# Kernel optimization log

Measured on AMD Instinct MI355X. Metric: run time of the kernel, lower is better.

## Reference

```python
import jax, jax.numpy as jnp
import numpy as np

D = 256
B, N1, N2 = 4, 512, 512


def setup_inputs() -> dict:
    key = jax.random.key(0)
    k = jax.random.split(key, 6)
    s1 = 1.0 / np.sqrt(2 * D)  # torch Linear init bound ~ U(-1/sqrt(fan_in), ...)
    s2 = 1.0 / np.sqrt(D)
    return {
        "x": jax.random.normal(k[0], (B, N1, D), jnp.float32),
        "y": jax.random.normal(k[1], (B, N2, D), jnp.float32),
        "W1": jax.random.uniform(k[2], (2 * D, D), jnp.float32, -s1, s1),  # linear1.weight.T
        "b1": jax.random.uniform(k[3], (D,), jnp.float32, -s1, s1),
        "W2": jax.random.uniform(k[4], (D, 1), jnp.float32, -s2, s2),  # out.weight.T
        "b2": jax.random.uniform(k[5], (1,), jnp.float32, -s2, s2),
    }


def reference(x, y, W1, b1, W2, b2):
    # linear1 over concat([x,y]) is separable: split W1 into x-part and y-part,
    # project each sequence once, then broadcast-sum over the (n1, n2) grid.
    Wx, Wy = W1[:D], W1[D:]                     # [d, d] each
    xp = jnp.einsum('bnd,de->bne', x, Wx)       # [b, n1, d]
    yp = jnp.einsum('bmd,de->bme', y, Wy)       # [b, n2, d]
    h = xp[:, :, None, :] + yp[:, None, :, :] + b1  # [b, n1, n2, d]
    h = jax.nn.gelu(h, approximate=False)       # torch nn.GELU() is exact erf
    o = jnp.einsum('bnmd,de->bnme', h, W2) + b2  # [b, n1, n2, 1]
    return o[..., 0]                             # [b, n1, n2]
```

## Files before the change

### kernel.cpp

```cpp
#include <hip/hip_runtime.h>

#define DD 256
#define N1 512
#define N2 512
#define BB 4

typedef float f2 __attribute__((ext_vector_type(2)));

__global__ __launch_bounds__(256) void proj_kernel(
    const float* __restrict__ x, const float* __restrict__ y,
    const float* __restrict__ W1, const float* __restrict__ b1,
    float* __restrict__ xp, float* __restrict__ yp)
{
    const int which = blockIdx.z;
    const float* __restrict__ A  = which ? y : x;
    const float* __restrict__ Bw = W1 + which * DD * DD;
    float* __restrict__ outp = which ? yp : xp;

    __shared__ float As[32 * 36];
    __shared__ float Bs[32 * 68];

    const int tid = threadIdx.x;
    const int tx = tid & 15, ty = tid >> 4;
    const int mBase = blockIdx.x * 32;
    const int nBase = blockIdx.y * 64;

    const float4* A4 = (const float4*)A;
    const float4* B4 = (const float4*)Bw;

    const int ar = tid >> 3;
    const int ac = tid & 7;
    const int br = tid >> 4;
    const int bc = tid & 15;

    float4 pa, pb0, pb1;
    pa  = A4[(mBase + ar) * 64 + ac];
    pb0 = B4[br * 64 + (nBase >> 2) + bc];
    pb1 = B4[(br + 16) * 64 + (nBase >> 2) + bc];

    float acc[2][4] = {};

    for (int kc = 0; kc < 8; ++kc) {
        __syncthreads();
        {
            float av[4] = {pa.x, pa.y, pa.z, pa.w};
            #pragma unroll
            for (int q = 0; q < 4; ++q) As[(ac * 4 + q) * 36 + ar] = av[q];
            *(float4*)&Bs[br * 68 + bc * 4] = pb0;
            *(float4*)&Bs[(br + 16) * 68 + bc * 4] = pb1;
        }
        __syncthreads();
        if (kc < 7) {
            pa  = A4[(mBase + ar) * 64 + (kc + 1) * 8 + ac];
            pb0 = B4[((kc + 1) * 32 + br) * 64 + (nBase >> 2) + bc];
            pb1 = B4[((kc + 1) * 32 + br + 16) * 64 + (nBase >> 2) + bc];
        }
        #pragma unroll
        for (int k = 0; k < 32; ++k) {
            float2 a = *(const float2*)&As[k * 36 + ty * 2];
            float4 b = *(const float4*)&Bs[k * 68 + tx * 4];
            float av[2] = {a.x, a.y};
            float bv[4] = {b.x, b.y, b.z, b.w};
            #pragma unroll
            for (int i = 0; i < 2; ++i)
                #pragma unroll
                for (int j = 0; j < 4; ++j)
                    acc[i][j] = fmaf(av[i], bv[j], acc[i][j]);
        }
    }

    float4 bias = make_float4(0.f, 0.f, 0.f, 0.f);
    if (which == 0) bias = *((const float4*)b1 + (nBase >> 2) + tx);
    #pragma unroll
    for (int i = 0; i < 2; ++i) {
        float4 o;
        o.x = acc[i][0] + bias.x;
        o.y = acc[i][1] + bias.y;
        o.z = acc[i][2] + bias.z;
        o.w = acc[i][3] + bias.w;
        ((float4*)outp)[(mBase + ty * 2 + i) * (DD / 4) + (nBase >> 2) + tx] = o;
    }
}

__device__ __forceinline__ f2 gelu2(f2 h)
{
    f2 h2 = h * h;
    f2 t  = __builtin_elementwise_fma(h2, (f2)0.1029432f, (f2)2.3022083f);
    f2 z  = h * t;
    f2 e;
    e.x = __builtin_amdgcn_exp2f(z.x);
    e.y = __builtin_amdgcn_exp2f(z.y);
    f2 a = e + 1.0f;
    f2 r;
    r.x = __int_as_float(0x7EF311C3 - __float_as_int(a.x));
    r.y = __int_as_float(0x7EF311C3 - __float_as_int(a.y));
    f2 w = __builtin_elementwise_fma(-a, r, (f2)2.0f);
    r = r * w;
    w = __builtin_elementwise_fma(-a, r, (f2)2.0f);
    r = r * w;
    return __builtin_elementwise_fma(-h, r, h);
}

__global__ __launch_bounds__(256, 4) void cross_kernel(
    const float* __restrict__ xp, const float* __restrict__ yp,
    const float* __restrict__ W2, const float* __restrict__ b2,
    float* __restrict__ o)
{
    __shared__ float xs[32 * 68];
    __shared__ float ys[32 * 68];

    const int tid   = threadIdx.x;
    const int b     = blockIdx.z;
    const int mBase = blockIdx.x * 32;
    const int nBase = blockIdx.y * 32;
    const int tx = tid & 15;
    const int ty = tid >> 4;

    const float4* xp4 = (const float4*)xp + (b * N1 + nBase) * (DD / 4);
    const float4* yp4 = (const float4*)yp + (b * N2 + mBase) * (DD / 4);
    const float4* __restrict__ W2v = (const float4*)W2;

    const int srow = tid >> 4;
    const int sc4  = tid & 15;

    float4 px[2], py[2];
    px[0] = xp4[srow * 64 + sc4];
    px[1] = xp4[(srow + 16) * 64 + sc4];
    py[0] = yp4[srow * 64 + sc4];
    py[1] = yp4[(srow + 16) * 64 + sc4];

    f2 acc[2][2] = {};

    for (int kc = 0; kc < 4; ++kc) {
        __syncthreads();
        *(float4*)&xs[srow * 68 + sc4 * 4]        = px[0];
        *(float4*)&xs[(srow + 16) * 68 + sc4 * 4] = px[1];
        *(float4*)&ys[srow * 68 + sc4 * 4]        = py[0];
        *(float4*)&ys[(srow + 16) * 68 + sc4 * 4] = py[1];
        __syncthreads();
        if (kc < 3) {
            px[0] = xp4[srow * 64 + (kc + 1) * 16 + sc4];
            px[1] = xp4[(srow + 16) * 64 + (kc + 1) * 16 + sc4];
            py[0] = yp4[srow * 64 + (kc + 1) * 16 + sc4];
            py[1] = yp4[(srow + 16) * 64 + (kc + 1) * 16 + sc4];
        }

        float4 wreg[16];
        #pragma unroll
        for (int c4 = 0; c4 < 16; ++c4) wreg[c4] = W2v[kc * 16 + c4];

        float4 xr[2][2], yr[2][2];
        #pragma unroll
        for (int i = 0; i < 2; ++i) {
            xr[0][i] = *(const float4*)&xs[(ty + 16 * i) * 68];
            yr[0][i] = *(const float4*)&ys[(tx + 16 * i) * 68];
        }

        #pragma unroll
        for (int c4 = 0; c4 < 16; ++c4) {
            const int cur = c4 & 1, nxt = cur ^ 1;
            if (c4 < 15) {
                #pragma unroll
                for (int i = 0; i < 2; ++i) {
                    xr[nxt][i] = *(const float4*)&xs[(ty + 16 * i) * 68 + (c4 + 1) * 4];
                    yr[nxt][i] = *(const float4*)&ys[(tx + 16 * i) * 68 + (c4 + 1) * 4];
                }
            }
            float4 wv = wreg[c4];
            f2 wlo = {wv.x, wv.y};
            f2 whi = {wv.z, wv.w};
            #pragma unroll
            for (int i = 0; i < 2; ++i) {
                f2 xlo = {xr[cur][i].x, xr[cur][i].y};
                f2 xhi = {xr[cur][i].z, xr[cur][i].w};
                #pragma unroll
                for (int j = 0; j < 2; ++j) {
                    f2 ylo = {yr[cur][j].x, yr[cur][j].y};
                    f2 yhi = {yr[cur][j].z, yr[cur][j].w};
                    f2 glo = gelu2(xlo + ylo);
                    acc[i][j] = __builtin_elementwise_fma(glo, wlo, acc[i][j]);
                    f2 ghi = gelu2(xhi + yhi);
                    acc[i][j] = __builtin_elementwise_fma(ghi, whi, acc[i][j]);
                }
            }
        }
    }

    const float bias2 = b2[0];
    const size_t base = ((size_t)(b * N1 + nBase)) * N2 + mBase;
    #pragma unroll
    for (int i = 0; i < 2; ++i) {
        #pragma unroll
        for (int j = 0; j < 2; ++j) {
            o[base + (size_t)(ty + 16 * i) * N2 + (tx + 16 * j)] =
                acc[i][j].x + acc[i][j].y + bias2;
        }
    }
}

extern "C" void kernel_launch(void* const* d_in, const int* in_sizes, int n_in,
                              void* d_out, int out_size, void* d_ws, size_t ws_size,
                              hipStream_t stream)
{
    const float* x  = (const float*)d_in[0];
    const float* y  = (const float*)d_in[1];
    const float* W1 = (const float*)d_in[2];
    const float* b1 = (const float*)d_in[3];
    const float* W2 = (const float*)d_in[4];
    const float* b2 = (const float*)d_in[5];
    float* o  = (float*)d_out;
    float* xp = (float*)d_ws;
    float* yp = xp + (BB * N1) * DD;

    dim3 g1(64, 4, 2);
    proj_kernel<<<g1, 256, 0, stream>>>(x, y, W1, b1, xp, yp);

    dim3 g2(N2 / 32, N1 / 32, BB);
    cross_kernel<<<g2, 256, 0, stream>>>(xp, yp, W2, b2, o);
}
```

Before: 153.8 us.

## Use hardware rcp in GELU and shrink cross-kernel tiles to 32x16

Replaces the bit-trick reciprocal plus two Newton iterations in the GELU approximation with a single hardware v_rcp_f32. This removes several VALU ops per element in the compute-bound inner loop, at some cost in precision. It also halves the cross kernel tile along N2 (128 threads, 32x16 outputs per block), which doubles the block count and changes the shared-memory staging and indexing. The smaller tiles reduce operand reuse per block and increase global loads of xp.

```diff
diff --git a/kernel.cpp b/kernel.cpp
--- a/kernel.cpp
+++ b/kernel.cpp
@@ -92,29 +92,25 @@
     e.y = __builtin_amdgcn_exp2f(z.y);
     f2 a = e + 1.0f;
     f2 r;
-    r.x = __int_as_float(0x7EF311C3 - __float_as_int(a.x));
-    r.y = __int_as_float(0x7EF311C3 - __float_as_int(a.y));
-    f2 w = __builtin_elementwise_fma(-a, r, (f2)2.0f);
-    r = r * w;
-    w = __builtin_elementwise_fma(-a, r, (f2)2.0f);
-    r = r * w;
+    r.x = __builtin_amdgcn_rcpf(a.x);
+    r.y = __builtin_amdgcn_rcpf(a.y);
     return __builtin_elementwise_fma(-h, r, h);
 }
 
-__global__ __launch_bounds__(256, 4) void cross_kernel(
+__global__ __launch_bounds__(128, 4) void cross_kernel(
     const float* __restrict__ xp, const float* __restrict__ yp,
     const float* __restrict__ W2, const float* __restrict__ b2,
     float* __restrict__ o)
 {
     __shared__ float xs[32 * 68];
-    __shared__ float ys[32 * 68];
+    __shared__ float ys[16 * 68];
 
     const int tid   = threadIdx.x;
     const int b     = blockIdx.z;
-    const int mBase = blockIdx.x * 32;
+    const int mBase = blockIdx.x * 16;
     const int nBase = blockIdx.y * 32;
-    const int tx = tid & 15;
-    const int ty = tid >> 4;
+    const int tx = tid & 7;
+    const int ty = tid >> 3;
 
     const float4* xp4 = (const float4*)xp + (b * N1 + nBase) * (DD / 4);
     const float4* yp4 = (const float4*)yp + (b * N2 + mBase) * (DD / 4);
@@ -123,26 +119,30 @@
     const int srow = tid >> 4;
     const int sc4  = tid & 15;
 
-    float4 px[2], py[2];
-    px[0] = xp4[srow * 64 + sc4];
-    px[1] = xp4[(srow + 16) * 64 + sc4];
-    py[0] = yp4[srow * 64 + sc4];
-    py[1] = yp4[(srow + 16) * 64 + sc4];
+    float4 px[4], py[2];
+    #pragma unroll
+    for (int t = 0; t < 4; ++t) px[t] = xp4[(srow + 8 * t) * 64 + sc4];
+    #pragma unroll
+    for (int t = 0; t < 2; ++t) py[t] = yp4[(srow + 8 * t) * 64 + sc4];
 
     f2 acc[2][2] = {};
 
     for (int kc = 0; kc < 4; ++kc) {
         __syncthreads();
-        *(float4*)&xs[srow * 68 + sc4 * 4]        = px[0];
-        *(float4*)&xs[(srow + 16) * 68 + sc4 * 4] = px[1];
-        *(float4*)&ys[srow * 68 + sc4 * 4]        = py[0];
-        *(float4*)&ys[(srow + 16) * 68 + sc4 * 4] = py[1];
+        #pragma unroll
+        for (int t = 0; t < 4; ++t)
+            *(float4*)&xs[(srow + 8 * t) * 68 + sc4 * 4] = px[t];
+        #pragma unroll
+        for (int t = 0; t < 2; ++t)
+            *(float4*)&ys[(srow + 8 * t) * 68 + sc4 * 4] = py[t];
         __syncthreads();
         if (kc < 3) {
-            px[0] = xp4[srow * 64 + (kc + 1) * 16 + sc4];
-            px[1] = xp4[(srow + 16) * 64 + (kc + 1) * 16 + sc4];
-            py[0] = yp4[srow * 64 + (kc + 1) * 16 + sc4];
-            py[1] = yp4[(srow + 16) * 64 + (kc + 1) * 16 + sc4];
+            #pragma unroll
+            for (int t = 0; t < 4; ++t)
+                px[t] = xp4[(srow + 8 * t) * 64 + (kc + 1) * 16 + sc4];
+            #pragma unroll
+            for (int t = 0; t < 2; ++t)
+                py[t] = yp4[(srow + 8 * t) * 64 + (kc + 1) * 16 + sc4];
         }
 
         float4 wreg[16];
@@ -153,7 +153,7 @@
         #pragma unroll
         for (int i = 0; i < 2; ++i) {
             xr[0][i] = *(const float4*)&xs[(ty + 16 * i) * 68];
-            yr[0][i] = *(const float4*)&ys[(tx + 16 * i) * 68];
+            yr[0][i] = *(const float4*)&ys[(tx + 8 * i) * 68];
         }
 
         #pragma unroll
@@ -163,7 +163,7 @@
                 #pragma unroll
                 for (int i = 0; i < 2; ++i) {
                     xr[nxt][i] = *(const float4*)&xs[(ty + 16 * i) * 68 + (c4 + 1) * 4];
-                    yr[nxt][i] = *(const float4*)&ys[(tx + 16 * i) * 68 + (c4 + 1) * 4];
+                    yr[nxt][i] = *(const float4*)&ys[(tx + 8 * i) * 68 + (c4 + 1) * 4];
                 }
             }
             float4 wv = wreg[c4];
@@ -192,7 +192,7 @@
     for (int i = 0; i < 2; ++i) {
         #pragma unroll
         for (int j = 0; j < 2; ++j) {
-            o[base + (size_t)(ty + 16 * i) * N2 + (tx + 16 * j)] =
+            o[base + (size_t)(ty + 16 * i) * N2 + (tx + 8 * j)] =
                 acc[i][j].x + acc[i][j].y + bias2;
         }
     }
@@ -215,6 +215,6 @@
     dim3 g1(64, 4, 2);
     proj_kernel<<<g1, 256, 0, stream>>>(x, y, W1, b1, xp, yp);
 
-    dim3 g2(N2 / 32, N1 / 32, BB);
-    cross_kernel<<<g2, 256, 0, stream>>>(xp, yp, W2, b2, o);
-}
+    dim3 g2(N2 / 16, N1 / 32, BB);
+    cross_kernel<<<g2, 128, 0, stream>>>(xp, yp, W2, b2, o);
+}
```

New measurement: 147.6 us. -4.0%, faster.
